# Kernel optimization log

Hardware: AMD Instinct MI355X
Metric: run time of the kernel (lower is better)

## Reference

```python
import jax, jax.numpy as jnp
import numpy as np

FOUR_PI = 4.0 * 3.14159265358979323846


def winding_numbers(points, tris):
    """Generalized winding number of `points` w.r.t. triangle soup `tris`.
    points: [B, P, 3]; tris: [B, F, 3, 3]. Returns [B, P].
    Uses the van Oosterom-Strackee solid-angle formula per triangle.
    """
    # relative vectors from each point to each triangle vertex: [B, P, F, 3, 3]
    r = tris[:, None, :, :, :] - points[:, :, None, None, :]
    a, b, c = r[..., 0, :], r[..., 1, :], r[..., 2, :]
    la = jnp.linalg.norm(a, axis=-1)
    lb = jnp.linalg.norm(b, axis=-1)
    lc = jnp.linalg.norm(c, axis=-1)
    det = jnp.sum(a * jnp.cross(b, c), axis=-1)
    denom = (la * lb * lc
             + jnp.sum(a * b, axis=-1) * lc
             + jnp.sum(b * c, axis=-1) * la
             + jnp.sum(c * a, axis=-1) * lb)
    omega = 2.0 * jnp.arctan2(det, denom)  # signed solid angle per triangle
    return jnp.sum(omega, axis=-1) / FOUR_PI  # [B, P]


def setup_inputs() -> dict:
    key = jax.random.key(0)
    k1, k2, k3, k4, k5 = jax.random.split(key, 5)
    B, V, Vs, F, LB = 4, 6890, 1024, 2048, 64
    vertices = jax.random.normal(k1, (B, V, 3), dtype=jnp.float32)
    segment_vidx = jax.random.randint(k2, (Vs,), 0, V).astype(jnp.int64)
    band0_idx = jax.random.randint(k3, (LB,), 0, V).astype(jnp.int64)
    band1_idx = jax.random.randint(k4, (LB,), 0, V).astype(jnp.int64)
    # closed mesh has V + 2 vertices (one appended mean vertex per band)
    segment_faces = jax.random.randint(k5, (F, 3), 0, V + 2).astype(jnp.int64)
    return {"vertices": vertices, "segment_vidx": segment_vidx,
            "band0_idx": band0_idx, "band1_idx": band1_idx,
            "segment_faces": segment_faces}


def reference(vertices, segment_vidx, band0_idx, band1_idx, segment_faces):
    # get_closed_segment: append the mean vertex of each boundary band
    b0 = jnp.mean(vertices[:, band0_idx, :], axis=1, keepdims=True)  # [B,1,3]
    b1 = jnp.mean(vertices[:, band1_idx, :], axis=1, keepdims=True)  # [B,1,3]
    segm_verts = jnp.concatenate([vertices, b0, b1], axis=1)         # [B,V+2,3]
    segm_triangles = segm_verts[:, segment_faces]                    # [B,F,3,3]
    pts = vertices[:, segment_vidx, :]                               # [B,Vs,3]
    wn = winding_numbers(pts, segm_triangles)                        # [B,Vs]
    # original: exterior = wn <= 0.99 (boolean); we return the float winding
    # numbers as the kernel-relevant output; threshold is a trivial epilogue.
    return wn
```

## Files before the change

### kernel.cpp

```cpp
#include <hip/hip_runtime.h>
#include <math.h>

#define INV_TWO_PI 0.15915494309189535f
#define PPB 4

__device__ __forceinline__ float fast_atan2f(float y, float x) {
    const float PI   = 3.14159265358979f;
    const float PI_2 = 1.57079632679490f;
    float ax = fabsf(x), ay = fabsf(y);
    float mx = fmaxf(ax, ay), mn = fminf(ax, ay);
    float inv = __builtin_amdgcn_rcpf(mx);
    float t = (mx > 0.f) ? mn * inv : 0.f;
    float s = t * t;
    float r = -0.0040540580f;
    r = fmaf(r, s, 0.0218612288f);
    r = fmaf(r, s, -0.0559098861f);
    r = fmaf(r, s, 0.0964200441f);
    r = fmaf(r, s, -0.1390853351f);
    r = fmaf(r, s, 0.1994653599f);
    r = fmaf(r, s, -0.3332985605f);
    r = fmaf(r, s, 0.9999993329f);
    r = r * t;
    if (ay > ax) r = PI_2 - r;
    if (x < 0.f) r = PI - r;
    return copysignf(r, y);
}

__device__ __forceinline__ float solid_angle_atan(
    float v0x, float v0y, float v0z,
    float v1x, float v1y, float v1z,
    float v2x, float v2y, float v2z,
    float px, float py, float pz) {
    float ax = v0x - px, ay = v0y - py, az = v0z - pz;
    float bx = v1x - px, by = v1y - py, bz = v1z - pz;
    float cx = v2x - px, cy = v2y - py, cz = v2z - pz;

    float la = __builtin_amdgcn_sqrtf(fmaf(ax, ax, fmaf(ay, ay, az * az)));
    float lb = __builtin_amdgcn_sqrtf(fmaf(bx, bx, fmaf(by, by, bz * bz)));
    float lc = __builtin_amdgcn_sqrtf(fmaf(cx, cx, fmaf(cy, cy, cz * cz)));

    float crx = by * cz - bz * cy;
    float cry = bz * cx - bx * cz;
    float crz = bx * cy - by * cx;
    float det = ax * crx + ay * cry + az * crz;

    float dab = fmaf(ax, bx, fmaf(ay, by, az * bz));
    float dbc = fmaf(bx, cx, fmaf(by, cy, bz * cz));
    float dca = fmaf(cx, ax, fmaf(cy, ay, cz * az));
    float den = fmaf(la * lb, lc, fmaf(dab, lc, fmaf(dbc, la, dca * lb)));

    return fast_atan2f(det, den);
}

__global__ __launch_bounds__(256) void winding_fused_kernel(
    const float* __restrict__ verts,
    const int* __restrict__ vidx,
    const int* __restrict__ b0i,
    const int* __restrict__ b1i,
    const int* __restrict__ faces,
    float* __restrict__ out,
    int P, int F, int V, int LB) {
    int nPB = (P + PPB - 1) / PPB;
    int b  = blockIdx.x / nPB;
    int pb = blockIdx.x - b * nPB;
    int p0 = pb * PPB;
    int tid = threadIdx.x;
    int wid = tid >> 6, lane = tid & 63;

    __shared__ float sband[6];
    if (wid < 2) {
        const int* bi = wid ? b1i : b0i;
        float sx = 0.f, sy = 0.f, sz = 0.f;
        for (int i = lane; i < LB; i += 64) {
            int vi = bi[i];
            const float* q = verts + ((size_t)b * V + vi) * 3;
            sx += q[0]; sy += q[1]; sz += q[2];
        }
#pragma unroll
        for (int off = 32; off; off >>= 1) {
            sx += __shfl_down(sx, off, 64);
            sy += __shfl_down(sy, off, 64);
            sz += __shfl_down(sz, off, 64);
        }
        if (lane == 0) {
            float inv = 1.0f / (float)LB;
            sband[wid * 3 + 0] = sx * inv;
            sband[wid * 3 + 1] = sy * inv;
            sband[wid * 3 + 2] = sz * inv;
        }
    }
    __syncthreads();

    float bnd[6];
#pragma unroll
    for (int c = 0; c < 6; ++c) bnd[c] = sband[c];

    float px[PPB], py[PPB], pz[PPB], acc[PPB];
#pragma unroll
    for (int j = 0; j < PPB; ++j) {
        int p = (p0 + j < P) ? (p0 + j) : (P - 1);
        const float* pt = verts + ((size_t)b * V + vidx[p]) * 3;
        px[j] = pt[0]; py[j] = pt[1]; pz[j] = pt[2];
        acc[j] = 0.f;
    }

    const float* vb = verts + (size_t)b * V * 3;
    for (int f = tid; f < F; f += 256) {
        int i0 = faces[f * 3 + 0];
        int i1 = faces[f * 3 + 1];
        int i2 = faces[f * 3 + 2];
        float v0x, v0y, v0z, v1x, v1y, v1z, v2x, v2y, v2z;
        if (i0 < V) { const float* s = vb + (size_t)i0 * 3; v0x = s[0]; v0y = s[1]; v0z = s[2]; }
        else { int j = (i0 - V) * 3; v0x = bnd[j]; v0y = bnd[j + 1]; v0z = bnd[j + 2]; }
        if (i1 < V) { const float* s = vb + (size_t)i1 * 3; v1x = s[0]; v1y = s[1]; v1z = s[2]; }
        else { int j = (i1 - V) * 3; v1x = bnd[j]; v1y = bnd[j + 1]; v1z = bnd[j + 2]; }
        if (i2 < V) { const float* s = vb + (size_t)i2 * 3; v2x = s[0]; v2y = s[1]; v2z = s[2]; }
        else { int j = (i2 - V) * 3; v2x = bnd[j]; v2y = bnd[j + 1]; v2z = bnd[j + 2]; }

#pragma unroll
        for (int j = 0; j < PPB; ++j) {
            acc[j] += solid_angle_atan(v0x, v0y, v0z, v1x, v1y, v1z,
                                       v2x, v2y, v2z, px[j], py[j], pz[j]);
        }
    }

#pragma unroll
    for (int off = 32; off; off >>= 1) {
#pragma unroll
        for (int j = 0; j < PPB; ++j) acc[j] += __shfl_down(acc[j], off, 64);
    }

    __shared__ float part[4][PPB];
    if ((tid & 63) == 0) {
#pragma unroll
        for (int j = 0; j < PPB; ++j) part[wid][j] = acc[j];
    }
    __syncthreads();
    if (tid < PPB) {
        int p = p0 + tid;
        if (p < P) {
            float tot = part[0][tid] + part[1][tid] + part[2][tid] + part[3][tid];
            out[(size_t)b * P + p] = tot * INV_TWO_PI;
        }
    }
}

extern "C" void kernel_launch(void* const* d_in, const int* in_sizes, int n_in,
                              void* d_out, int out_size, void* d_ws, size_t ws_size,
                              hipStream_t stream) {
    const float* verts = (const float*)d_in[0];
    const int* svidx   = (const int*)d_in[1];
    const int* b0i     = (const int*)d_in[2];
    const int* b1i     = (const int*)d_in[3];
    const int* faces   = (const int*)d_in[4];
    float* out = (float*)d_out;

    int P  = in_sizes[1];
    int LB = in_sizes[2];
    int F  = in_sizes[4] / 3;
    int B  = out_size / P;
    int V  = in_sizes[0] / (3 * B);

    int nPB = (P + PPB - 1) / PPB;
    winding_fused_kernel<<<B * nPB, 256, 0, stream>>>(verts, svidx, b0i, b1i,
                                                      faces, out, P, F, V, LB);
    (void)d_ws; (void)ws_size; (void)n_in;
}
```

Measured before the change: 88.42 us.

## Pre-gather triangle vertices into workspace and prefetch them in winding kernel

Adds a separate kernel that resolves face indices and band-mean vertices once per batch, writing packed triangles (12 floats, float4-aligned) into the workspace. The winding kernel then streams these contiguous triangles with vector loads and software-prefetches the next triangle while computing the current one. This removes the repeated per-block index lookups, scattered vertex gathers and band-mean recomputation. In exchange it adds a second launch and a workspace round trip. The band-mean reduction now runs in every gather block instead of every winding block.

Result: faster. 81.02 us (-8.4%).

```diff
diff --git a/kernel.cpp b/kernel.cpp
--- a/kernel.cpp
+++ b/kernel.cpp
@@ -2,7 +2,6 @@
 #include <math.h>
 
 #define INV_TWO_PI 0.15915494309189535f
-#define PPB 4
 
 __device__ __forceinline__ float fast_atan2f(float y, float x) {
     const float PI   = 3.14159265358979f;
@@ -52,18 +51,14 @@
     return fast_atan2f(det, den);
 }
 
-__global__ __launch_bounds__(256) void winding_fused_kernel(
-    const float* __restrict__ verts,
-    const int* __restrict__ vidx,
-    const int* __restrict__ b0i,
-    const int* __restrict__ b1i,
-    const int* __restrict__ faces,
-    float* __restrict__ out,
-    int P, int F, int V, int LB) {
-    int nPB = (P + PPB - 1) / PPB;
-    int b  = blockIdx.x / nPB;
-    int pb = blockIdx.x - b * nPB;
-    int p0 = pb * PPB;
+__global__ void gather_tris_kernel(const float* __restrict__ verts,
+                                   const int* __restrict__ b0i,
+                                   const int* __restrict__ b1i,
+                                   const int* __restrict__ faces,
+                                   float* __restrict__ tri,
+                                   int B, int V, int F, int LB, int nfc) {
+    int b  = blockIdx.x / nfc;
+    int fc = blockIdx.x - b * nfc;
     int tid = threadIdx.x;
     int wid = tid >> 6, lane = tid & 63;
 
@@ -91,57 +86,110 @@
     }
     __syncthreads();
 
-    float bnd[6];
-#pragma unroll
-    for (int c = 0; c < 6; ++c) bnd[c] = sband[c];
-
-    float px[PPB], py[PPB], pz[PPB], acc[PPB];
-#pragma unroll
-    for (int j = 0; j < PPB; ++j) {
-        int p = (p0 + j < P) ? (p0 + j) : (P - 1);
-        const float* pt = verts + ((size_t)b * V + vidx[p]) * 3;
-        px[j] = pt[0]; py[j] = pt[1]; pz[j] = pt[2];
-        acc[j] = 0.f;
-    }
-
-    const float* vb = verts + (size_t)b * V * 3;
-    for (int f = tid; f < F; f += 256) {
-        int i0 = faces[f * 3 + 0];
-        int i1 = faces[f * 3 + 1];
-        int i2 = faces[f * 3 + 2];
-        float v0x, v0y, v0z, v1x, v1y, v1z, v2x, v2y, v2z;
-        if (i0 < V) { const float* s = vb + (size_t)i0 * 3; v0x = s[0]; v0y = s[1]; v0z = s[2]; }
-        else { int j = (i0 - V) * 3; v0x = bnd[j]; v0y = bnd[j + 1]; v0z = bnd[j + 2]; }
-        if (i1 < V) { const float* s = vb + (size_t)i1 * 3; v1x = s[0]; v1y = s[1]; v1z = s[2]; }
-        else { int j = (i1 - V) * 3; v1x = bnd[j]; v1y = bnd[j + 1]; v1z = bnd[j + 2]; }
-        if (i2 < V) { const float* s = vb + (size_t)i2 * 3; v2x = s[0]; v2y = s[1]; v2z = s[2]; }
-        else { int j = (i2 - V) * 3; v2x = bnd[j]; v2y = bnd[j + 1]; v2z = bnd[j + 2]; }
-
-#pragma unroll
-        for (int j = 0; j < PPB; ++j) {
-            acc[j] += solid_angle_atan(v0x, v0y, v0z, v1x, v1y, v1z,
-                                       v2x, v2y, v2z, px[j], py[j], pz[j]);
-        }
+    int f = fc * 256 + tid;
+    if (f >= F) return;
+
+    int i0 = faces[f * 3 + 0];
+    int i1 = faces[f * 3 + 1];
+    int i2 = faces[f * 3 + 2];
+    float v0x, v0y, v0z, v1x, v1y, v1z, v2x, v2y, v2z;
+    if (i0 < V) { const float* s = verts + ((size_t)b * V + i0) * 3; v0x = s[0]; v0y = s[1]; v0z = s[2]; }
+    else { int j = (i0 - V) * 3; v0x = sband[j]; v0y = sband[j + 1]; v0z = sband[j + 2]; }
+    if (i1 < V) { const float* s = verts + ((size_t)b * V + i1) * 3; v1x = s[0]; v1y = s[1]; v1z = s[2]; }
+    else { int j = (i1 - V) * 3; v1x = sband[j]; v1y = sband[j + 1]; v1z = sband[j + 2]; }
+    if (i2 < V) { const float* s = verts + ((size_t)b * V + i2) * 3; v2x = s[0]; v2y = s[1]; v2z = s[2]; }
+    else { int j = (i2 - V) * 3; v2x = sband[j]; v2y = sband[j + 1]; v2z = sband[j + 2]; }
+
+    float4* d = (float4*)(tri + ((size_t)b * F + f) * 12);
+    d[0] = make_float4(v0x, v0y, v0z, v1x);
+    d[1] = make_float4(v1y, v1z, v2x, v2y);
+    d[2] = make_float4(v2z, 0.f, 0.f, 0.f);
+}
+
+__global__ __launch_bounds__(256) void winding4_kernel(
+    const float* __restrict__ tri,
+    const float* __restrict__ verts,
+    const int* __restrict__ vidx,
+    float* __restrict__ out,
+    int P, int F, int V) {
+    int nPB = (P + 3) / 4;
+    int b  = blockIdx.x / nPB;
+    int pb = blockIdx.x - b * nPB;
+    int p0 = pb * 4;
+    int tid = threadIdx.x;
+
+    const float4* tb = (const float4*)(tri + (size_t)b * F * 12);
+
+    int f = tid;
+    float4 q0 = make_float4(0.f, 0.f, 0.f, 0.f), q1 = q0, q2 = q0;
+    if (f < F) {
+        q0 = tb[(size_t)f * 3 + 0];
+        q1 = tb[(size_t)f * 3 + 1];
+        q2 = tb[(size_t)f * 3 + 2];
+    }
+
+    const float* vbase = verts + (size_t)b * V * 3;
+    int pc0 = (p0 + 0 < P) ? (p0 + 0) : (P - 1);
+    int pc1 = (p0 + 1 < P) ? (p0 + 1) : (P - 1);
+    int pc2 = (p0 + 2 < P) ? (p0 + 2) : (P - 1);
+    int pc3 = (p0 + 3 < P) ? (p0 + 3) : (P - 1);
+    const float* pt0 = vbase + (size_t)vidx[pc0] * 3;
+    const float* pt1 = vbase + (size_t)vidx[pc1] * 3;
+    const float* pt2 = vbase + (size_t)vidx[pc2] * 3;
+    const float* pt3 = vbase + (size_t)vidx[pc3] * 3;
+    float px0 = pt0[0], py0 = pt0[1], pz0 = pt0[2];
+    float px1 = pt1[0], py1 = pt1[1], pz1 = pt1[2];
+    float px2 = pt2[0], py2 = pt2[1], pz2 = pt2[2];
+    float px3 = pt3[0], py3 = pt3[1], pz3 = pt3[2];
+    float acc0 = 0.f, acc1 = 0.f, acc2 = 0.f, acc3 = 0.f;
+
+    while (f < F) {
+        int fn = f + 256;
+        float4 n0 = q0, n1 = q1, n2 = q2;
+        if (fn < F) {
+            n0 = tb[(size_t)fn * 3 + 0];
+            n1 = tb[(size_t)fn * 3 + 1];
+            n2 = tb[(size_t)fn * 3 + 2];
+        }
+        acc0 += solid_angle_atan(q0.x, q0.y, q0.z, q0.w, q1.x, q1.y,
+                                 q1.z, q1.w, q2.x, px0, py0, pz0);
+        acc1 += solid_angle_atan(q0.x, q0.y, q0.z, q0.w, q1.x, q1.y,
+                                 q1.z, q1.w, q2.x, px1, py1, pz1);
+        acc2 += solid_angle_atan(q0.x, q0.y, q0.z, q0.w, q1.x, q1.y,
+                                 q1.z, q1.w, q2.x, px2, py2, pz2);
+        acc3 += solid_angle_atan(q0.x, q0.y, q0.z, q0.w, q1.x, q1.y,
+                                 q1.z, q1.w, q2.x, px3, py3, pz3);
+        q0 = n0; q1 = n1; q2 = n2;
+        f = fn;
     }
 
 #pragma unroll
     for (int off = 32; off; off >>= 1) {
-#pragma unroll
-        for (int j = 0; j < PPB; ++j) acc[j] += __shfl_down(acc[j], off, 64);
-    }
-
-    __shared__ float part[4][PPB];
+        acc0 += __shfl_down(acc0, off, 64);
+        acc1 += __shfl_down(acc1, off, 64);
+        acc2 += __shfl_down(acc2, off, 64);
+        acc3 += __shfl_down(acc3, off, 64);
+    }
+
+    __shared__ float part0[4], part1[4], part2[4], part3[4];
+    int wid = tid >> 6;
     if ((tid & 63) == 0) {
-#pragma unroll
-        for (int j = 0; j < PPB; ++j) part[wid][j] = acc[j];
+        part0[wid] = acc0;
+        part1[wid] = acc1;
+        part2[wid] = acc2;
+        part3[wid] = acc3;
     }
     __syncthreads();
-    if (tid < PPB) {
-        int p = p0 + tid;
-        if (p < P) {
-            float tot = part[0][tid] + part[1][tid] + part[2][tid] + part[3][tid];
-            out[(size_t)b * P + p] = tot * INV_TWO_PI;
-        }
+    if (tid == 0) {
+        float t0 = part0[0] + part0[1] + part0[2] + part0[3];
+        float t1 = part1[0] + part1[1] + part1[2] + part1[3];
+        float t2 = part2[0] + part2[1] + part2[2] + part2[3];
+        float t3 = part3[0] + part3[1] + part3[2] + part3[3];
+        float* o = out + (size_t)b * P + p0;
+        if (p0 + 0 < P) o[0] = t0 * INV_TWO_PI;
+        if (p0 + 1 < P) o[1] = t1 * INV_TWO_PI;
+        if (p0 + 2 < P) o[2] = t2 * INV_TWO_PI;
+        if (p0 + 3 < P) o[3] = t3 * INV_TWO_PI;
     }
 }
 
@@ -161,8 +209,10 @@
     int B  = out_size / P;
     int V  = in_sizes[0] / (3 * B);
 
-    int nPB = (P + PPB - 1) / PPB;
-    winding_fused_kernel<<<B * nPB, 256, 0, stream>>>(verts, svidx, b0i, b1i,
-                                                      faces, out, P, F, V, LB);
-    (void)d_ws; (void)ws_size; (void)n_in;
-}
+    float* tri = (float*)d_ws;
+    int nfc = (F + 255) / 256;
+    gather_tris_kernel<<<B * nfc, 256, 0, stream>>>(verts, b0i, b1i, faces,
+                                                    tri, B, V, F, LB, nfc);
+    int nPB = (P + 3) / 4;
+    winding4_kernel<<<B * nPB, 256, 0, stream>>>(tri, verts, svidx, out, P, F, V);
+}
```
